# Performance work log

Measured on AMD Instinct MI355X. Metric: run time of the kernel, lower is better.

## Reference

```python
import jax, jax.numpy as jnp
import numpy as np

D_MODEL = 1024
N_HEADS = 16
D_HEAD = D_MODEL // N_HEADS
WINDOW = 256
SCALE = D_HEAD ** -0.5


def setup_inputs() -> dict:
    key = jax.random.key(0)
    ks = jax.random.split(key, 5)
    B, S = 2, 2048
    x = jax.random.normal(ks[0], (B, S, D_MODEL), dtype=jnp.float32)
    # weights stored as [d_in, d_out] so forward is x @ W + b
    W_qkv = jax.random.normal(ks[1], (D_MODEL, 3 * D_MODEL), dtype=jnp.float32) * (D_MODEL ** -0.5)
    b_qkv = jnp.zeros((3 * D_MODEL,), dtype=jnp.float32)
    W_out = jax.random.normal(ks[2], (D_MODEL, D_MODEL), dtype=jnp.float32) * (D_MODEL ** -0.5)
    b_out = jnp.zeros((D_MODEL,), dtype=jnp.float32)
    return {"x": x, "W_qkv": W_qkv, "b_qkv": b_qkv, "W_out": W_out, "b_out": b_out}


def _window_mask(S):
    # Faithful to source: keep positions where (i <= j) & (i >= j - WINDOW + 1),
    # i = query index (rows), j = key index (cols). (Anti-causal window, as in repo.)
    idx = jnp.arange(S)
    keep = (idx[:, None] <= idx[None, :]) & (idx[:, None] >= idx[None, :] - WINDOW + 1)
    return keep  # [S, S] bool


def reference(x, W_qkv, b_qkv, W_out, b_out):
    B, S, D = x.shape
    qkv = x @ W_qkv + b_qkv                      # [B,S,3D]
    q, k, v = jnp.split(qkv, 3, axis=-1)
    def heads(t):
        return t.reshape(B, S, N_HEADS, D_HEAD).transpose(0, 2, 1, 3)  # [B,H,S,dh]
    q, k, v = heads(q), heads(k), heads(v)
    attn = jnp.einsum('bhid,bhjd->bhij', q, k) * SCALE  # [B,H,S,S]
    keep = _window_mask(S)
    attn = jnp.where(keep[None, None], attn, -jnp.inf)
    attn = jax.nn.softmax(attn, axis=-1)
    # dropout is identity in eval mode
    out = jnp.einsum('bhij,bhjd->bhid', attn, v)        # [B,H,S,dh]
    out = out.transpose(0, 2, 1, 3).reshape(B, S, D)
    return out @ W_out + b_out
```

## Files before the change

### kernel.cpp

```cpp
#include <hip/hip_runtime.h>

typedef __bf16 bf16x8 __attribute__((ext_vector_type(8)));
typedef float f32x4 __attribute__((ext_vector_type(4)));
typedef unsigned short u16x8 __attribute__((ext_vector_type(8)));
typedef unsigned short u16x4 __attribute__((ext_vector_type(4)));

#define MFMA16(a, b, c) __builtin_amdgcn_mfma_f32_16x16x32_bf16((a), (b), (c), 0, 0, 0)

__device__ __forceinline__ unsigned short f2bf(float f) {
  union { float f; unsigned int i; } v; v.f = f;
  unsigned int u = v.i;
  u += 0x7fffu + ((u >> 16) & 1u);
  return (unsigned short)(u >> 16);
}

__device__ __forceinline__ void gload16(const void* g, void* l) {
  __builtin_amdgcn_global_load_lds(
      (const __attribute__((address_space(1))) unsigned int*)g,
      (__attribute__((address_space(3))) unsigned int*)l, 16, 0, 0);
}

__global__ __launch_bounds__(256) void convert_x(const float* __restrict__ X,
                                                 unsigned short* __restrict__ Xb) {
  size_t i = (size_t)(blockIdx.x * 256 + threadIdx.x) * 8;
  f32x4 f0 = *(const f32x4*)(X + i);
  f32x4 f1 = *(const f32x4*)(X + i + 4);
  u16x8 t;
#pragma unroll
  for (int j = 0; j < 4; ++j) { t[j] = f2bf(f0[j]); t[4 + j] = f2bf(f1[j]); }
  *(u16x8*)(Xb + i) = t;
}

__global__ __launch_bounds__(256) void transpose_w(const float* __restrict__ W,
                                                   unsigned short* __restrict__ Wt,
                                                   int N) {
  __shared__ unsigned short t[32][33];
  int tx = threadIdx.x & 31, ty = threadIdx.x >> 5;
  int bx = blockIdx.x;
  int by = blockIdx.y;
#pragma unroll
  for (int j = 0; j < 4; ++j) {
    int r = ty + j * 8;
    t[tx][r] = f2bf(W[(size_t)(by * 32 + r) * N + bx * 32 + tx]);
  }
  __syncthreads();
#pragma unroll
  for (int j = 0; j < 4; ++j) {
    int r = ty + j * 8;
    Wt[(size_t)(bx * 32 + r) * 1024 + by * 32 + tx] = t[r][tx];
  }
}

__global__ __launch_bounds__(256) void gemm_bt(
    const unsigned short* __restrict__ A, const unsigned short* __restrict__ Bt,
    const float* __restrict__ bias,
    unsigned short* __restrict__ O0, unsigned short* __restrict__ O1,
    unsigned short* __restrict__ O2, float* __restrict__ OF, int mode) {
  __shared__ __align__(16) unsigned short As0[128 * 32];
  __shared__ __align__(16) unsigned short Bs0[128 * 32];
  __shared__ __align__(16) unsigned short As1[128 * 32];
  __shared__ __align__(16) unsigned short Bs1[128 * 32];

  const int K = 1024;
  int tid = threadIdx.x;
  int lane = tid & 63, wave = tid >> 6, quad = lane >> 4, l16 = lane & 15;
  int wrow = wave >> 1, wcol = wave & 1;

  int gx = gridDim.x;
  int nwg = gx * gridDim.y;
  int lin = blockIdx.y * gx + blockIdx.x;
  int swz = (lin & 7) * (nwg >> 3) + (lin >> 3);
  int m0 = (swz % gx) * 128, n0 = (swz / gx) * 128;

  const unsigned short* ag[2]; const unsigned short* bg[2];
  int loff[2];
#pragma unroll
  for (int i = 0; i < 2; ++i) {
    int c = tid + 256 * i, row = c >> 2, u = c & 3;
    ag[i] = A + (size_t)(m0 + row) * K + u * 8;
    bg[i] = Bt + (size_t)(n0 + row) * K + u * 8;
    loff[i] = c * 16;
  }

  int abase = (wrow * 64 + l16) * 64 + quad * 16;
  int bbase = (wcol * 64 + l16) * 64 + quad * 16;

  f32x4 acc[4][4];
#pragma unroll
  for (int i = 0; i < 4; ++i)
#pragma unroll
    for (int j = 0; j < 4; ++j) acc[i][j] = f32x4{0.f, 0.f, 0.f, 0.f};

  auto STAGE = [&](int k0, char* Asb, char* Bsb) {
#pragma unroll
    for (int i = 0; i < 2; ++i) {
      gload16(ag[i] + k0, Asb + loff[i]);
      gload16(bg[i] + k0, Bsb + loff[i]);
    }
  };
  auto COMPUTE = [&](const char* Asb, const char* Bsb) {
    bf16x8 af[4], bfr[4];
#pragma unroll
    for (int t = 0; t < 4; ++t) {
      af[t]  = *(const bf16x8*)(Asb + abase + t * 1024);
      bfr[t] = *(const bf16x8*)(Bsb + bbase + t * 1024);
    }
#pragma unroll
    for (int mt = 0; mt < 4; ++mt)
#pragma unroll
      for (int nt = 0; nt < 4; ++nt)
        acc[mt][nt] = MFMA16(af[mt], bfr[nt], acc[mt][nt]);
  };
#define WAIT_VM4  asm volatile("s_waitcnt vmcnt(4)" ::: "memory")
#define WAIT_VM0  asm volatile("s_waitcnt vmcnt(0)" ::: "memory")
#define WAIT_LGKM asm volatile("s_waitcnt lgkmcnt(0)" ::: "memory")
#define BAR       __builtin_amdgcn_s_barrier()

  STAGE(0, (char*)As0, (char*)Bs0);
  for (int t = 0; t < 30; t += 2) {
    STAGE((t + 1) * 32, (char*)As1, (char*)Bs1);
    WAIT_VM4; BAR;
    COMPUTE((const char*)As0, (const char*)Bs0);
    WAIT_LGKM; BAR;
    STAGE((t + 2) * 32, (char*)As0, (char*)Bs0);
    WAIT_VM4; BAR;
    COMPUTE((const char*)As1, (const char*)Bs1);
    WAIT_LGKM; BAR;
  }
  STAGE(31 * 32, (char*)As1, (char*)Bs1);
  WAIT_VM4; BAR;
  COMPUTE((const char*)As0, (const char*)Bs0);
  WAIT_LGKM; BAR;
  WAIT_VM0; BAR;
  COMPUTE((const char*)As1, (const char*)Bs1);

  if (mode == 0) {
#pragma unroll
    for (int nt = 0; nt < 4; ++nt) {
      int n = n0 + wcol * 64 + nt * 16 + l16;
      float bv = bias[n];
      int seg = n >> 10, cc = n & 1023, hh = cc >> 6, d = cc & 63;
#pragma unroll
      for (int mt = 0; mt < 4; ++mt) {
        int mb = m0 + wrow * 64 + mt * 16 + quad * 4;
        int b = mb >> 11, s = mb & 2047;
        if (seg == 2) {
          u16x4 pk;
#pragma unroll
          for (int r = 0; r < 4; ++r) pk[r] = f2bf(acc[mt][nt][r] + bv);
          *(u16x4*)&O2[((size_t)((b << 4) + hh) * 64 + d) * 2048 + s] = pk;
        } else {
          unsigned short* O = seg ? O1 : O0;
#pragma unroll
          for (int r = 0; r < 4; ++r)
            O[((size_t)((b << 4) + hh) * 2048 + (s + r)) * 64 + d] = f2bf(acc[mt][nt][r] + bv);
        }
      }
    }
  } else {
#pragma unroll
    for (int nt = 0; nt < 4; ++nt) {
      int n = n0 + wcol * 64 + nt * 16 + l16;
      float bv = bias[n];
#pragma unroll
      for (int mt = 0; mt < 4; ++mt) {
        int mb = m0 + wrow * 64 + mt * 16 + quad * 4;
#pragma unroll
        for (int r = 0; r < 4; ++r)
          OF[(size_t)(mb + r) * 1024 + n] = acc[mt][nt][r] + bv;
      }
    }
  }
}

__global__ __launch_bounds__(256) void attn_kernel(
    const unsigned short* __restrict__ Q, const unsigned short* __restrict__ Kq,
    const unsigned short* __restrict__ Vt, unsigned short* __restrict__ AO) {
  __shared__ __align__(16) unsigned short Ks[32][72];
  __shared__ __align__(16) unsigned short Vs[64][40];
  __shared__ __align__(16) unsigned short Ps[4][16][40];

  int bid = blockIdx.x;
  int qblk = bid & 31, h = (bid >> 5) & 15, b = bid >> 9;
  int q0 = qblk * 64;
  int tid = threadIdx.x, lane = tid & 63, wave = tid >> 6, quad = lane >> 4, l16 = lane & 15;

  const unsigned short* Qb = Q + (size_t)(((b << 4) + h) * 2048) * 64;
  const unsigned short* Kb = Kq + (size_t)(((b << 4) + h) * 2048) * 64;
  const unsigned short* Vb = Vt + (size_t)(((b << 4) + h) * 64) * 2048;

  int qrow = q0 + wave * 16 + l16;
  bf16x8 qf0 = __builtin_bit_cast(bf16x8, *(const u16x8*)&Qb[(size_t)qrow * 64 + quad * 8]);
  bf16x8 qf1 = __builtin_bit_cast(bf16x8, *(const u16x8*)&Qb[(size_t)qrow * 64 + 32 + quad * 8]);

  float mrow[4], lrow[4];
  f32x4 zero = {0.f, 0.f, 0.f, 0.f};
  f32x4 o[4];
#pragma unroll
  for (int i = 0; i < 4; ++i) o[i] = zero;
#pragma unroll
  for (int r = 0; r < 4; ++r) { mrow[r] = -1e30f; lrow[r] = 0.f; }

  const float SCALE = 0.125f;
  int pstart = (wave >= 2) ? 1 : 0;
  int pend = pstart + 8;

  int ki = tid >> 3, kc = (tid & 7) * 8;
  int vd = tid >> 2, vc = (tid & 3) * 8;

  for (int p = 0; p < 10; ++p) {
    int kbase = q0 + p * 32;
    {
      int s = kbase + ki; s = s > 2047 ? 2047 : s;
      *(u16x8*)&Ks[ki][kc] = *(const u16x8*)&Kb[(size_t)s * 64 + kc];
    }
    if (kbase + vc + 7 <= 2047) {
      *(u16x8*)&Vs[vd][vc] = *(const u16x8*)&Vb[(size_t)vd * 2048 + kbase + vc];
    } else {
#pragma unroll
      for (int j = 0; j < 8; ++j) {
        int s = kbase + vc + j; s = s > 2047 ? 2047 : s;
        Vs[vd][vc + j] = Vb[(size_t)vd * 2048 + s];
      }
    }
    __syncthreads();

    if (p >= pstart && p <= pend) {
      f32x4 sc[2];
#pragma unroll
      for (int t = 0; t < 2; ++t) {
        bf16x8 kf0 = __builtin_bit_cast(bf16x8, *(const u16x8*)&Ks[t * 16 + l16][quad * 8]);
        bf16x8 kf1 = __builtin_bit_cast(bf16x8, *(const u16x8*)&Ks[t * 16 + l16][32 + quad * 8]);
        f32x4 z = zero;
        z = MFMA16(qf0, kf0, z);
        z = MFMA16(qf1, kf1, z);
        sc[t] = z;
      }
      float sv[2][4];
#pragma unroll
      for (int t = 0; t < 2; ++t)
#pragma unroll
        for (int r = 0; r < 4; ++r) {
          int kg = kbase + t * 16 + l16;
          int qg = q0 + wave * 16 + quad * 4 + r;
          bool valid = (kg >= qg) && (kg <= qg + 255) && (kg < 2048);
          sv[t][r] = valid ? sc[t][r] * SCALE : -1e30f;
        }
#pragma unroll
      for (int r = 0; r < 4; ++r) {
        float v = fmaxf(sv[0][r], sv[1][r]);
        v = fmaxf(v, __shfl_xor(v, 1));
        v = fmaxf(v, __shfl_xor(v, 2));
        v = fmaxf(v, __shfl_xor(v, 4));
        v = fmaxf(v, __shfl_xor(v, 8));
        float mnew = fmaxf(mrow[r], v);
        float alpha = __expf(mrow[r] - mnew);
        mrow[r] = mnew;
        float p0 = __expf(sv[0][r] - mnew);
        float p1 = __expf(sv[1][r] - mnew);
        p0 = (sv[0][r] > -5e29f) ? p0 : 0.f;
        p1 = (sv[1][r] > -5e29f) ? p1 : 0.f;
        float rs = p0 + p1;
        rs += __shfl_xor(rs, 1);
        rs += __shfl_xor(rs, 2);
        rs += __shfl_xor(rs, 4);
        rs += __shfl_xor(rs, 8);
        lrow[r] = lrow[r] * alpha + rs;
#pragma unroll
        for (int nt = 0; nt < 4; ++nt) o[nt][r] *= alpha;
        Ps[wave][quad * 4 + r][l16] = f2bf(p0);
        Ps[wave][quad * 4 + r][16 + l16] = f2bf(p1);
      }
      __threadfence_block();
      bf16x8 pf = __builtin_bit_cast(bf16x8, *(const u16x8*)&Ps[wave][l16][quad * 8]);
#pragma unroll
      for (int nt = 0; nt < 4; ++nt) {
        bf16x8 vf = __builtin_bit_cast(bf16x8, *(const u16x8*)&Vs[nt * 16 + l16][quad * 8]);
        o[nt] = MFMA16(pf, vf, o[nt]);
      }
    }
    __syncthreads();
  }

  unsigned short* dst = AO + ((size_t)(b * 2048 + q0 + wave * 16) * 1024) + h * 64;
#pragma unroll
  for (int nt = 0; nt < 4; ++nt)
#pragma unroll
    for (int r = 0; r < 4; ++r) {
      int qq = quad * 4 + r;
      dst[(size_t)qq * 1024 + nt * 16 + l16] = f2bf(o[nt][r] / lrow[r]);
    }
}

extern "C" void kernel_launch(void* const* d_in, const int* in_sizes, int n_in,
                              void* d_out, int out_size, void* d_ws, size_t ws_size,
                              hipStream_t stream) {
  const float* x = (const float*)d_in[0];
  const float* W_qkv = (const float*)d_in[1];
  const float* b_qkv = (const float*)d_in[2];
  const float* W_out = (const float*)d_in[3];
  const float* b_out = (const float*)d_in[4];
  float* out = (float*)d_out;

  unsigned short* ws = (unsigned short*)d_ws;
  unsigned short* Qw  = ws;
  unsigned short* Kw  = ws + 4194304;
  unsigned short* Vw  = ws + 8388608;
  unsigned short* Wqt = ws + 12582912;
  unsigned short* AO  = ws + 12582912;
  unsigned short* Wot = ws;
  unsigned short* Xb  = (unsigned short*)d_out;

  dim3 blk(256);
  convert_x<<<dim3(2048), blk, 0, stream>>>(x, Xb);
  transpose_w<<<dim3(96, 32), blk, 0, stream>>>(W_qkv, Wqt, 3072);
  gemm_bt<<<dim3(32, 24), blk, 0, stream>>>(Xb, Wqt, b_qkv, Qw, Kw, Vw, nullptr, 0);
  attn_kernel<<<dim3(1024), blk, 0, stream>>>(Qw, Kw, Vw, AO);
  transpose_w<<<dim3(32, 32), blk, 0, stream>>>(W_out, Wot, 1024);
  gemm_bt<<<dim3(32, 8), blk, 0, stream>>>(AO, Wot, b_out, nullptr, nullptr, nullptr, out, 1);
}
```

Measured before the change: 176.6 us.

## Use 512-thread GEMM blocks with 8 waves per 128x128 tile, drop grid swizzle

The GEMM workgroup grows from 4 to 8 waves. Each wave now computes a 64x32 sub-tile instead of 64x64, and each thread issues one async global-to-LDS load per operand per stage instead of two, so the vmcnt waits drop accordingly. The L2-locality block swizzle is removed in favour of direct blockIdx mapping. The goal is more latency hiding through more waves. The cost is fewer MFMAs per LDS fragment load, which lowers register reuse, and possibly worse cache locality without the swizzle.

```diff
diff --git a/kernel.cpp b/kernel.cpp
--- a/kernel.cpp
+++ b/kernel.cpp
@@ -51,7 +51,7 @@
   }
 }
 
-__global__ __launch_bounds__(256) void gemm_bt(
+__global__ __launch_bounds__(512) void gemm_bt(
     const unsigned short* __restrict__ A, const unsigned short* __restrict__ Bt,
     const float* __restrict__ bias,
     unsigned short* __restrict__ O0, unsigned short* __restrict__ O1,
@@ -64,54 +64,42 @@
   const int K = 1024;
   int tid = threadIdx.x;
   int lane = tid & 63, wave = tid >> 6, quad = lane >> 4, l16 = lane & 15;
-  int wrow = wave >> 1, wcol = wave & 1;
-
-  int gx = gridDim.x;
-  int nwg = gx * gridDim.y;
-  int lin = blockIdx.y * gx + blockIdx.x;
-  int swz = (lin & 7) * (nwg >> 3) + (lin >> 3);
-  int m0 = (swz % gx) * 128, n0 = (swz / gx) * 128;
-
-  const unsigned short* ag[2]; const unsigned short* bg[2];
-  int loff[2];
-#pragma unroll
-  for (int i = 0; i < 2; ++i) {
-    int c = tid + 256 * i, row = c >> 2, u = c & 3;
-    ag[i] = A + (size_t)(m0 + row) * K + u * 8;
-    bg[i] = Bt + (size_t)(n0 + row) * K + u * 8;
-    loff[i] = c * 16;
-  }
-
-  int abase = (wrow * 64 + l16) * 64 + quad * 16;
-  int bbase = (wcol * 64 + l16) * 64 + quad * 16;
-
-  f32x4 acc[4][4];
+  int wr = wave >> 2, wc = wave & 3;
+  int m0 = blockIdx.x * 128, n0 = blockIdx.y * 128;
+
+  int srow = tid >> 2, su = tid & 3;
+  const unsigned short* ag = A + (size_t)(m0 + srow) * K + su * 8;
+  const unsigned short* bg = Bt + (size_t)(n0 + srow) * K + su * 8;
+  int loff = tid * 16;
+
+  int abase = (wr * 64 + l16) * 64 + quad * 16;
+  int bbase = (wc * 32 + l16) * 64 + quad * 16;
+
+  f32x4 acc[4][2];
 #pragma unroll
   for (int i = 0; i < 4; ++i)
 #pragma unroll
-    for (int j = 0; j < 4; ++j) acc[i][j] = f32x4{0.f, 0.f, 0.f, 0.f};
+    for (int j = 0; j < 2; ++j) acc[i][j] = f32x4{0.f, 0.f, 0.f, 0.f};
 
   auto STAGE = [&](int k0, char* Asb, char* Bsb) {
-#pragma unroll
-    for (int i = 0; i < 2; ++i) {
-      gload16(ag[i] + k0, Asb + loff[i]);
-      gload16(bg[i] + k0, Bsb + loff[i]);
-    }
+    gload16(ag + k0, Asb + loff);
+    gload16(bg + k0, Bsb + loff);
   };
   auto COMPUTE = [&](const char* Asb, const char* Bsb) {
-    bf16x8 af[4], bfr[4];
-#pragma unroll
-    for (int t = 0; t < 4; ++t) {
-      af[t]  = *(const bf16x8*)(Asb + abase + t * 1024);
+    bf16x8 af[4], bfr[2];
+#pragma unroll
+    for (int t = 0; t < 4; ++t)
+      af[t] = *(const bf16x8*)(Asb + abase + t * 1024);
+#pragma unroll
+    for (int t = 0; t < 2; ++t)
       bfr[t] = *(const bf16x8*)(Bsb + bbase + t * 1024);
-    }
 #pragma unroll
     for (int mt = 0; mt < 4; ++mt)
 #pragma unroll
-      for (int nt = 0; nt < 4; ++nt)
+      for (int nt = 0; nt < 2; ++nt)
         acc[mt][nt] = MFMA16(af[mt], bfr[nt], acc[mt][nt]);
   };
-#define WAIT_VM4  asm volatile("s_waitcnt vmcnt(4)" ::: "memory")
+#define WAIT_VM2  asm volatile("s_waitcnt vmcnt(2)" ::: "memory")
 #define WAIT_VM0  asm volatile("s_waitcnt vmcnt(0)" ::: "memory")
 #define WAIT_LGKM asm volatile("s_waitcnt lgkmcnt(0)" ::: "memory")
 #define BAR       __builtin_amdgcn_s_barrier()
@@ -119,16 +107,16 @@
   STAGE(0, (char*)As0, (char*)Bs0);
   for (int t = 0; t < 30; t += 2) {
     STAGE((t + 1) * 32, (char*)As1, (char*)Bs1);
-    WAIT_VM4; BAR;
+    WAIT_VM2; BAR;
     COMPUTE((const char*)As0, (const char*)Bs0);
     WAIT_LGKM; BAR;
     STAGE((t + 2) * 32, (char*)As0, (char*)Bs0);
-    WAIT_VM4; BAR;
+    WAIT_VM2; BAR;
     COMPUTE((const char*)As1, (const char*)Bs1);
     WAIT_LGKM; BAR;
   }
   STAGE(31 * 32, (char*)As1, (char*)Bs1);
-  WAIT_VM4; BAR;
+  WAIT_VM2; BAR;
   COMPUTE((const char*)As0, (const char*)Bs0);
   WAIT_LGKM; BAR;
   WAIT_VM0; BAR;
@@ -136,13 +124,13 @@
 
   if (mode == 0) {
 #pragma unroll
-    for (int nt = 0; nt < 4; ++nt) {
-      int n = n0 + wcol * 64 + nt * 16 + l16;
+    for (int nt = 0; nt < 2; ++nt) {
+      int n = n0 + wc * 32 + nt * 16 + l16;
       float bv = bias[n];
       int seg = n >> 10, cc = n & 1023, hh = cc >> 6, d = cc & 63;
 #pragma unroll
       for (int mt = 0; mt < 4; ++mt) {
-        int mb = m0 + wrow * 64 + mt * 16 + quad * 4;
+        int mb = m0 + wr * 64 + mt * 16 + quad * 4;
         int b = mb >> 11, s = mb & 2047;
         if (seg == 2) {
           u16x4 pk;
@@ -159,12 +147,12 @@
     }
   } else {
 #pragma unroll
-    for (int nt = 0; nt < 4; ++nt) {
-      int n = n0 + wcol * 64 + nt * 16 + l16;
+    for (int nt = 0; nt < 2; ++nt) {
+      int n = n0 + wc * 32 + nt * 16 + l16;
       float bv = bias[n];
 #pragma unroll
       for (int mt = 0; mt < 4; ++mt) {
-        int mb = m0 + wrow * 64 + mt * 16 + quad * 4;
+        int mb = m0 + wr * 64 + mt * 16 + quad * 4;
 #pragma unroll
         for (int r = 0; r < 4; ++r)
           OF[(size_t)(mb + r) * 1024 + n] = acc[mt][nt][r] + bv;
@@ -312,10 +300,11 @@
   unsigned short* Xb  = (unsigned short*)d_out;
 
   dim3 blk(256);
+  dim3 gblk(512);
   convert_x<<<dim3(2048), blk, 0, stream>>>(x, Xb);
   transpose_w<<<dim3(96, 32), blk, 0, stream>>>(W_qkv, Wqt, 3072);
-  gemm_bt<<<dim3(32, 24), blk, 0, stream>>>(Xb, Wqt, b_qkv, Qw, Kw, Vw, nullptr, 0);
+  gemm_bt<<<dim3(32, 24), gblk, 0, stream>>>(Xb, Wqt, b_qkv, Qw, Kw, Vw, nullptr, 0);
   attn_kernel<<<dim3(1024), blk, 0, stream>>>(Qw, Kw, Vw, AO);
   transpose_w<<<dim3(32, 32), blk, 0, stream>>>(W_out, Wot, 1024);
-  gemm_bt<<<dim3(32, 8), blk, 0, stream>>>(AO, Wot, b_out, nullptr, nullptr, nullptr, out, 1);
-}
+  gemm_bt<<<dim3(32, 8), gblk, 0, stream>>>(AO, Wot, b_out, nullptr, nullptr, nullptr, out, 1);
+}
```

Measured after the change: 170.2 us. 3.6% less time.
